# Optimization experiments

Measured on AMD Instinct MI355X. Metric: run time of the kernel, lower is better.

The kernel has to match this reference:

```python
import jax, jax.numpy as jnp
import numpy as np

TEMPERATURE = 0.5
EPS = 1e-20


def setup_inputs() -> dict:
    key = jax.random.key(0)
    ks = jax.random.split(key, 7)
    N, T, S = 16, 64, 1024
    SRC, TGT, D = 512, 512, 64
    return {
        "input": jax.random.normal(ks[0], (N, T, TGT), jnp.float32),
        "memory_bank": jax.random.normal(ks[1], (N, S, SRC), jnp.float32),
        "W_q": jax.random.normal(ks[2], (TGT, D), jnp.float32) / np.sqrt(TGT),
        "W_ctx": jax.random.normal(ks[3], (SRC, D), jnp.float32) / np.sqrt(SRC),
        "v": jax.random.normal(ks[4], (D,), jnp.float32) / np.sqrt(D),
        "W_out": jax.random.normal(ks[5], (SRC + TGT, TGT), jnp.float32) / np.sqrt(SRC + TGT),
        "b_out": jax.random.normal(ks[6], (TGT,), jnp.float32) * 0.01,
    }


def reference(input, memory_bank, W_q, W_ctx, v, W_out, b_out):
    # MLP attention score: v^T tanh(W_q q + W_ctx h)
    wq = jnp.einsum("ntd,de->nte", input, W_q)            # [N,T,D]
    uh = jnp.einsum("nsd,de->nse", memory_bank, W_ctx)    # [N,S,D]
    wquh = jnp.tanh(wq[:, :, None, :] + uh[:, None, :, :])  # [N,T,S,D]
    scores = jnp.einsum("ntsd,d->nts", wquh, v)           # [N,T,S]

    log_alpha = jax.nn.log_softmax(scores, axis=-1)
    alpha = jnp.exp(log_alpha)                            # c_align_vectors

    # deterministic context + output
    context_c = jnp.einsum("nts,nsd->ntd", alpha, memory_bank)
    h_c = jnp.tanh(jnp.concatenate([input, context_c], axis=-1) @ W_out + b_out)

    # gumbel-softmax sample (K = n_samples = 1, forced by view_as in original)
    u = jax.random.uniform(jax.random.key(42), log_alpha.shape, jnp.float32)
    g = -jnp.log(-jnp.log(u + EPS) + EPS)                 # gumbel noise
    y_align = jax.nn.softmax((log_alpha + g) / TEMPERATURE, axis=-1)  # [N,T,S]

    context_y = jnp.einsum("nts,nsd->ntd", y_align, memory_bank)
    h_y = jnp.tanh(jnp.concatenate([input, context_y], axis=-1) @ W_out + b_out)

    return jnp.stack([h_c, h_y], axis=0)  # [2,N,T,tgt_dim]
```

## Files before the change

### kernel.cpp

```cpp
#include <hip/hip_runtime.h>
#include <hip/hip_bf16.h>
#include <stdint.h>

#define DEV __device__ __forceinline__

typedef __attribute__((ext_vector_type(8))) short short8;
typedef __attribute__((ext_vector_type(4))) float f32x4;

#define TWO_LOG2E 2.8853900817779268f

DEV unsigned short f2bf(float f) {
  uint32_t u = __float_as_uint(f);
  u += 0x7FFFu + ((u >> 16) & 1u);
  return (unsigned short)(u >> 16);
}

DEV uint2 pk4(float4 f) {
  union { __hip_bfloat162 h; unsigned u; } a, b;
  a.h = __float22bfloat162_rn(make_float2(f.x, f.y));
  b.h = __float22bfloat162_rn(make_float2(f.z, f.w));
  return make_uint2(a.u, b.u);
}

DEV short8 mk8(uint2 lo, uint2 hi) {
  union { short8 s; uint4 u; } t;
  t.u = make_uint4(lo.x, lo.y, hi.x, hi.y);
  return t.s;
}

DEV uint32_t rotl32(uint32_t x, int r) { return (x << r) | (x >> (32 - r)); }

DEV void threefry_0_42(uint32_t x0, uint32_t x1, uint32_t& o0, uint32_t& o1) {
  const uint32_t ks0 = 0u, ks1 = 42u, ks2 = 0x1BD11BDAu ^ 42u;
  x0 += ks0; x1 += ks1;
#define TFR(r) { x0 += x1; x1 = rotl32(x1, (r)); x1 ^= x0; }
  TFR(13) TFR(15) TFR(26) TFR(6)  x0 += ks1; x1 += ks2 + 1u;
  TFR(17) TFR(29) TFR(16) TFR(24) x0 += ks2; x1 += ks0 + 2u;
  TFR(13) TFR(15) TFR(26) TFR(6)  x0 += ks0; x1 += ks1 + 3u;
  TFR(17) TFR(29) TFR(16) TFR(24) x0 += ks1; x1 += ks2 + 4u;
  TFR(13) TFR(15) TFR(26) TFR(6)  x0 += ks2; x1 += ks0 + 5u;
#undef TFR
  o0 = x0; o1 = x1;
}

DEV float wredmax(float v) {
#pragma unroll
  for (int off = 32; off > 0; off >>= 1) v = fmaxf(v, __shfl_xor(v, off));
  return v;
}
DEV float wredsum(float v) {
#pragma unroll
  for (int off = 32; off > 0; off >>= 1) v += __shfl_xor(v, off);
  return v;
}

__global__ __launch_bounds__(256) void transpose_all(const float* __restrict__ Wctx,
                                                     const float* __restrict__ Wq,
                                                     const float* __restrict__ Wout,
                                                     unsigned short* __restrict__ WctxT,
                                                     unsigned short* __restrict__ WqT,
                                                     unsigned short* __restrict__ WoutT) {
  __shared__ float tile[64][65];
  const int b = blockIdx.x;
  const float* src; unsigned short* dst; int R, C, br, bc;
  if (b < 8)       { src = Wctx; dst = WctxT; R = 512;  C = 64;  br = b * 64;        bc = 0; }
  else if (b < 16) { src = Wq;   dst = WqT;   R = 512;  C = 64;  br = (b - 8) * 64;  bc = 0; }
  else { int i = b - 16; src = Wout; dst = WoutT; R = 1024; C = 512; br = (i & 15) * 64; bc = (i >> 4) * 64; }
  const int tid = threadIdx.x;
  const int lr = tid >> 4, lc4 = (tid & 15) * 4;
#pragma unroll
  for (int i = 0; i < 4; ++i) {
    float4 v = *(const float4*)(src + (long)(br + lr + i * 16) * C + bc + lc4);
    tile[lr + i * 16][lc4 + 0] = v.x;
    tile[lr + i * 16][lc4 + 1] = v.y;
    tile[lr + i * 16][lc4 + 2] = v.z;
    tile[lr + i * 16][lc4 + 3] = v.w;
  }
  __syncthreads();
#pragma unroll
  for (int i = 0; i < 4; ++i) {
    int crow = lr + i * 16;
    ushort4 o;
    o.x = f2bf(tile[lc4 + 0][crow]);
    o.y = f2bf(tile[lc4 + 1][crow]);
    o.z = f2bf(tile[lc4 + 2][crow]);
    o.w = f2bf(tile[lc4 + 3][crow]);
    *(ushort4*)(dst + (long)(bc + crow) * R + br + lc4) = o;
  }
}

__global__ __launch_bounds__(256) void gemm_uhwq(const float* __restrict__ mb,
                                                 const float* __restrict__ input,
                                                 const unsigned short* __restrict__ WctxT,
                                                 const unsigned short* __restrict__ WqT,
                                                 float* __restrict__ uh,
                                                 float* __restrict__ wqo) {
  __shared__ unsigned short As[64][32];
  __shared__ unsigned short Bs[64][32];
  const int tid = threadIdx.x;
  const int bx = blockIdx.x;
  const float* A;  const unsigned short* BT;  float* C;  int mbase;
  if (bx < 256) { A = mb;    BT = WctxT; C = uh;  mbase = bx * 64; }
  else          { A = input; BT = WqT;   C = wqo; mbase = (bx - 256) * 64; }
  const int srow = tid >> 2, kc = tid & 3;
  const int scol = ((kc ^ (srow & 3)) * 8);
  const int wave = tid >> 6, lane = tid & 63;
  const int wm = (wave >> 1) * 32, wn = (wave & 1) * 32;
  const int q = lane >> 4, r = lane & 15;
  const int c0 = ((q ^ (r & 3)) * 8);
  const float* ap = A + (long)(mbase + srow) * 512 + kc * 8;
  const unsigned short* bp = BT + (long)srow * 512 + kc * 8;
  f32x4 acc[2][2];
#pragma unroll
  for (int i = 0; i < 2; ++i)
#pragma unroll
    for (int j = 0; j < 2; ++j) acc[i][j] = (f32x4){0.f, 0.f, 0.f, 0.f};

  float4 fa0 = *(const float4*)(ap);
  float4 fa1 = *(const float4*)(ap + 4);
  uint4 fb = *(const uint4*)(bp);
  for (int k0 = 0; k0 < 512; k0 += 32) {
    uint2 p0 = pk4(fa0), p1 = pk4(fa1);
    *(uint4*)&As[srow][scol] = make_uint4(p0.x, p0.y, p1.x, p1.y);
    *(uint4*)&Bs[srow][scol] = fb;
    __syncthreads();
    if (k0 + 32 < 512) {
      fa0 = *(const float4*)(ap + k0 + 32);
      fa1 = *(const float4*)(ap + k0 + 36);
      fb = *(const uint4*)(bp + k0 + 32);
    }
    short8 a0 = *(const short8*)&As[wm + r][c0];
    short8 a1 = *(const short8*)&As[wm + 16 + r][c0];
    short8 b0 = *(const short8*)&Bs[wn + r][c0];
    short8 b1 = *(const short8*)&Bs[wn + 16 + r][c0];
    acc[0][0] = __builtin_amdgcn_mfma_f32_16x16x32_bf16(a0, b0, acc[0][0], 0, 0, 0);
    acc[0][1] = __builtin_amdgcn_mfma_f32_16x16x32_bf16(a0, b1, acc[0][1], 0, 0, 0);
    acc[1][0] = __builtin_amdgcn_mfma_f32_16x16x32_bf16(a1, b0, acc[1][0], 0, 0, 0);
    acc[1][1] = __builtin_amdgcn_mfma_f32_16x16x32_bf16(a1, b1, acc[1][1], 0, 0, 0);
    __syncthreads();
  }
#pragma unroll
  for (int i2 = 0; i2 < 2; ++i2)
#pragma unroll
    for (int j2 = 0; j2 < 2; ++j2) {
      int gcol = wn + j2 * 16 + r;
#pragma unroll
      for (int reg = 0; reg < 4; ++reg) {
        int grow = mbase + wm + i2 * 16 + q * 4 + reg;
        C[(long)grow * 64 + gcol] = acc[i2][j2][reg] * TWO_LOG2E;
      }
    }
}

__global__ __launch_bounds__(256) void gemm_ctx_mfma(const float* __restrict__ alpha,
                                                     const float* __restrict__ yal,
                                                     const float* __restrict__ mb,
                                                     float* __restrict__ ctx) {
  __shared__ unsigned short As[64][32];
  const int tid = threadIdx.x;
  const int vt = blockIdx.x >> 4, n = blockIdx.x & 15;
  const int dbase = blockIdx.y * 32;
  const int srow = tid >> 2, kc = tid & 3;
  const int scol = ((kc ^ (srow & 3)) * 8);
  const int wave = tid >> 6, lane = tid & 63;
  const int wm = (wave >> 1) * 32, wn = (wave & 1) * 16;
  const int q = lane >> 4, r = lane & 15;
  const int c0 = ((q ^ (r & 3)) * 8);
  const float* Abase = (vt == 0 ? alpha : yal) + (long)n * 65536;
  const float* ap = Abase + (long)srow * 1024 + kc * 8;
  const float* bcol = mb + (long)n * 524288 + dbase + wn + r;
  f32x4 acc[2];
  acc[0] = (f32x4){0.f, 0.f, 0.f, 0.f};
  acc[1] = (f32x4){0.f, 0.f, 0.f, 0.f};

  float4 fa0 = *(const float4*)(ap);
  float4 fa1 = *(const float4*)(ap + 4);
  float bv[8];
#pragma unroll
  for (int j = 0; j < 8; ++j) bv[j] = bcol[(long)(q * 8 + j) * 512];

  for (int k0 = 0; k0 < 1024; k0 += 32) {
    uint2 p0 = pk4(fa0), p1 = pk4(fa1);
    *(uint4*)&As[srow][scol] = make_uint4(p0.x, p0.y, p1.x, p1.y);
    __syncthreads();
    float4 blo = make_float4(bv[0], bv[1], bv[2], bv[3]);
    float4 bhi = make_float4(bv[4], bv[5], bv[6], bv[7]);
    short8 b0 = mk8(pk4(blo), pk4(bhi));
    if (k0 + 32 < 1024) {
      fa0 = *(const float4*)(ap + k0 + 32);
      fa1 = *(const float4*)(ap + k0 + 36);
#pragma unroll
      for (int j = 0; j < 8; ++j) bv[j] = bcol[(long)(k0 + 32 + q * 8 + j) * 512];
    }
    short8 a0 = *(const short8*)&As[wm + r][c0];
    short8 a1 = *(const short8*)&As[wm + 16 + r][c0];
    acc[0] = __builtin_amdgcn_mfma_f32_16x16x32_bf16(a0, b0, acc[0], 0, 0, 0);
    acc[1] = __builtin_amdgcn_mfma_f32_16x16x32_bf16(a1, b0, acc[1], 0, 0, 0);
    __syncthreads();
  }
#pragma unroll
  for (int i2 = 0; i2 < 2; ++i2) {
    int gcol = dbase + wn + r;
#pragma unroll
    for (int reg = 0; reg < 4; ++reg) {
      long grow = (long)vt * 1024 + n * 64 + wm + i2 * 16 + q * 4 + reg;
      ctx[grow * 512 + gcol] = acc[i2][reg];
    }
  }
}

__global__ __launch_bounds__(256) void gemm_out_mfma(const float* __restrict__ input,
                                                     const float* __restrict__ ctx,
                                                     const unsigned short* __restrict__ WoutT,
                                                     const float* __restrict__ bout,
                                                     float* __restrict__ out) {
  __shared__ unsigned short As[64][32];
  __shared__ unsigned short Bs[64][32];
  const int tid = threadIdx.x;
  const int mbase = blockIdx.x * 64, nbase = blockIdx.y * 64;
  const int srow = tid >> 2, kc = tid & 3;
  const int scol = ((kc ^ (srow & 3)) * 8);
  const int wave = tid >> 6, lane = tid & 63;
  const int wm = (wave >> 1) * 32, wn = (wave & 1) * 32;
  const int q = lane >> 4, r = lane & 15;
  const int c0 = ((q ^ (r & 3)) * 8);
  const int vv = mbase >> 10, nt = (mbase + srow) & 1023;
  const float* ap_lo = input + (long)nt * 512 + kc * 8;
  const float* ap_hi = ctx + (long)(vv * 1024 + nt) * 512 + kc * 8 - 512;
  const unsigned short* bp = WoutT + (long)(nbase + srow) * 1024 + kc * 8;
  f32x4 acc[2][2];
#pragma unroll
  for (int i = 0; i < 2; ++i)
#pragma unroll
    for (int j = 0; j < 2; ++j) acc[i][j] = (f32x4){0.f, 0.f, 0.f, 0.f};

  float4 fa0 = *(const float4*)(ap_lo);
  float4 fa1 = *(const float4*)(ap_lo + 4);
  uint4 fb = *(const uint4*)(bp);
  for (int k0 = 0; k0 < 1024; k0 += 32) {
    uint2 p0 = pk4(fa0), p1 = pk4(fa1);
    *(uint4*)&As[srow][scol] = make_uint4(p0.x, p0.y, p1.x, p1.y);
    *(uint4*)&Bs[srow][scol] = fb;
    __syncthreads();
    int kn = k0 + 32;
    if (kn < 1024) {
      const float* apn = (kn < 512) ? ap_lo : ap_hi;
      fa0 = *(const float4*)(apn + kn);
      fa1 = *(const float4*)(apn + kn + 4);
      fb = *(const uint4*)(bp + kn);
    }
    short8 a0 = *(const short8*)&As[wm + r][c0];
    short8 a1 = *(const short8*)&As[wm + 16 + r][c0];
    short8 b0 = *(const short8*)&Bs[wn + r][c0];
    short8 b1 = *(const short8*)&Bs[wn + 16 + r][c0];
    acc[0][0] = __builtin_amdgcn_mfma_f32_16x16x32_bf16(a0, b0, acc[0][0], 0, 0, 0);
    acc[0][1] = __builtin_amdgcn_mfma_f32_16x16x32_bf16(a0, b1, acc[0][1], 0, 0, 0);
    acc[1][0] = __builtin_amdgcn_mfma_f32_16x16x32_bf16(a1, b0, acc[1][0], 0, 0, 0);
    acc[1][1] = __builtin_amdgcn_mfma_f32_16x16x32_bf16(a1, b1, acc[1][1], 0, 0, 0);
    __syncthreads();
  }
#pragma unroll
  for (int i2 = 0; i2 < 2; ++i2)
#pragma unroll
    for (int j2 = 0; j2 < 2; ++j2) {
      int gcol = nbase + wn + j2 * 16 + r;
      float bb = bout[gcol];
#pragma unroll
      for (int reg = 0; reg < 4; ++reg) {
        int grow = mbase + wm + i2 * 16 + q * 4 + reg;
        float z = acc[i2][j2][reg] + bb;
        float rc = __builtin_amdgcn_rcpf(1.f + __builtin_amdgcn_exp2f(z * TWO_LOG2E));
        out[(long)grow * 512 + gcol] = fmaf(-2.f, rc, 1.f);
      }
    }
}

__global__ __launch_bounds__(256) void scores_kernel(const float* __restrict__ uh2,
                                                     const float* __restrict__ wq2,
                                                     const float* __restrict__ v,
                                                     float* __restrict__ alpha_g,
                                                     float* __restrict__ y_g) {
  const int tid = threadIdx.x;
  const int nt = blockIdx.x;
  const int n = nt >> 6;
  __shared__ float wvs[64];
  __shared__ float vvs[64];
  __shared__ float red[4];
  if (tid < 64) {
    wvs[tid] = wq2[nt * 64 + tid];
    vvs[tid] = v[tid];
  }
  __syncthreads();

  float sumv = 0.f;
#pragma unroll
  for (int d = 0; d < 64; d += 4) {
    float4 vv = *(const float4*)&vvs[d];
    sumv += vv.x + vv.y + vv.z + vv.w;
  }

  const float* un = uh2 + (long)n * 65536;
  float lsc[4];
#pragma unroll
  for (int i = 0; i < 4; ++i) {
    const float* up = un + (long)(i * 256 + tid) * 64;
    float racc = 0.f;
#pragma unroll
    for (int dc = 0; dc < 16; ++dc) {
      float4 u = *(const float4*)(up + dc * 4);
      float4 w = *(const float4*)&wvs[dc * 4];
      float4 vv = *(const float4*)&vvs[dc * 4];
      racc = fmaf(vv.x, __builtin_amdgcn_rcpf(1.f + __builtin_amdgcn_exp2f(u.x + w.x)), racc);
      racc = fmaf(vv.y, __builtin_amdgcn_rcpf(1.f + __builtin_amdgcn_exp2f(u.y + w.y)), racc);
      racc = fmaf(vv.z, __builtin_amdgcn_rcpf(1.f + __builtin_amdgcn_exp2f(u.z + w.z)), racc);
      racc = fmaf(vv.w, __builtin_amdgcn_rcpf(1.f + __builtin_amdgcn_exp2f(u.w + w.w)), racc);
    }
    lsc[i] = fmaf(-2.f, racc, sumv);
  }

  const int wv = tid >> 6, ln = tid & 63;
  float m = fmaxf(fmaxf(lsc[0], lsc[1]), fmaxf(lsc[2], lsc[3]));
  m = wredmax(m);
  if (ln == 0) red[wv] = m;
  __syncthreads();
  m = fmaxf(fmaxf(red[0], red[1]), fmaxf(red[2], red[3]));
  __syncthreads();
  float ss = 0.f;
#pragma unroll
  for (int i = 0; i < 4; ++i) ss += __expf(lsc[i] - m);
  ss = wredsum(ss);
  if (ln == 0) red[wv] = ss;
  __syncthreads();
  ss = red[0] + red[1] + red[2] + red[3];
  const float logl = __logf(ss);
  __syncthreads();

  float ys[4];
#pragma unroll
  for (int i = 0; i < 4; ++i) {
    int s = tid + 256 * i;
    float la = lsc[i] - m - logl;
    alpha_g[(long)nt * 1024 + s] = __expf(la);
    uint32_t j = (uint32_t)nt * 1024u + (uint32_t)s;
    uint32_t o0, o1;
    threefry_0_42(0u, j, o0, o1);
    uint32_t bits = o0 ^ o1;
    float u = __uint_as_float((bits >> 9) | 0x3f800000u) - 1.0f;
    float g = -__logf(-__logf(u + 1e-20f) + 1e-20f);
    ys[i] = (la + g) * 2.0f;
  }

  float m2 = fmaxf(fmaxf(ys[0], ys[1]), fmaxf(ys[2], ys[3]));
  m2 = wredmax(m2);
  if (ln == 0) red[wv] = m2;
  __syncthreads();
  m2 = fmaxf(fmaxf(red[0], red[1]), fmaxf(red[2], red[3]));
  __syncthreads();
  float s2 = 0.f;
  float ye[4];
#pragma unroll
  for (int i = 0; i < 4; ++i) { ye[i] = __expf(ys[i] - m2); s2 += ye[i]; }
  s2 = wredsum(s2);
  if (ln == 0) red[wv] = s2;
  __syncthreads();
  s2 = red[0] + red[1] + red[2] + red[3];
  const float rinv = __fdividef(1.f, s2);
#pragma unroll
  for (int i = 0; i < 4; ++i) y_g[(long)nt * 1024 + tid + 256 * i] = ye[i] * rinv;
}

extern "C" void kernel_launch(void* const* d_in, const int* in_sizes, int n_in,
                              void* d_out, int out_size, void* d_ws, size_t ws_size,
                              hipStream_t stream) {
  const float* input = (const float*)d_in[0];
  const float* mb    = (const float*)d_in[1];
  const float* W_q   = (const float*)d_in[2];
  const float* W_ctx = (const float*)d_in[3];
  const float* v     = (const float*)d_in[4];
  const float* W_out = (const float*)d_in[5];
  const float* b_out = (const float*)d_in[6];
  float* out = (float*)d_out;
  float* ws = (float*)d_ws;

  float* uh    = ws;
  float* wq    = ws + 1048576;
  float* yal   = ws + 1114112;
  unsigned short* WctxT = (unsigned short*)(ws + 2162688);
  unsigned short* WqT   = (unsigned short*)(ws + 2179072);
  unsigned short* WoutT = (unsigned short*)(ws + 2195456);
  float* alpha = out;
  float* ctx   = uh;

  transpose_all<<<144, 256, 0, stream>>>(W_ctx, W_q, W_out, WctxT, WqT, WoutT);
  gemm_uhwq<<<272, 256, 0, stream>>>(mb, input, WctxT, WqT, uh, wq);
  scores_kernel<<<1024, 256, 0, stream>>>(uh, wq, v, alpha, yal);
  gemm_ctx_mfma<<<dim3(32, 16), 256, 0, stream>>>(alpha, yal, mb, ctx);
  gemm_out_mfma<<<dim3(32, 8), 256, 0, stream>>>(input, ctx, WoutT, b_out, out);
}
```

Baseline: 177.6 us.

## Store uh transposed for coalesced score reads and halve output GEMM N-tile

The uh GEMM now writes its result transposed as [N][D][S], so the scores kernel can have each thread handle four consecutive s positions. Each d-row then becomes a coalesced float4 load, replacing the strided per-row reads of 64 floats. The alpha and y writes become float4 stores, and the threefry counters are remapped to match. Separately, the output GEMM uses a 32-wide N tile with a doubled grid to raise the block count, at the cost of more A-tile reloads and idle B-loading threads.

```diff
diff --git a/kernel.cpp b/kernel.cpp
--- a/kernel.cpp
+++ b/kernel.cpp
@@ -93,15 +93,15 @@
                                                  const float* __restrict__ input,
                                                  const unsigned short* __restrict__ WctxT,
                                                  const unsigned short* __restrict__ WqT,
-                                                 float* __restrict__ uh,
+                                                 float* __restrict__ uhT,
                                                  float* __restrict__ wqo) {
   __shared__ unsigned short As[64][32];
   __shared__ unsigned short Bs[64][32];
   const int tid = threadIdx.x;
   const int bx = blockIdx.x;
-  const float* A;  const unsigned short* BT;  float* C;  int mbase;
-  if (bx < 256) { A = mb;    BT = WctxT; C = uh;  mbase = bx * 64; }
-  else          { A = input; BT = WqT;   C = wqo; mbase = (bx - 256) * 64; }
+  const float* A;  const unsigned short* BT;  int mbase;
+  if (bx < 256) { A = mb;    BT = WctxT; mbase = bx * 64; }
+  else          { A = input; BT = WqT;   mbase = (bx - 256) * 64; }
   const int srow = tid >> 2, kc = tid & 3;
   const int scol = ((kc ^ (srow & 3)) * 8);
   const int wave = tid >> 6, lane = tid & 63;
@@ -144,10 +144,19 @@
 #pragma unroll
     for (int j2 = 0; j2 < 2; ++j2) {
       int gcol = wn + j2 * 16 + r;
-#pragma unroll
-      for (int reg = 0; reg < 4; ++reg) {
-        int grow = mbase + wm + i2 * 16 + q * 4 + reg;
-        C[(long)grow * 64 + gcol] = acc[i2][j2][reg] * TWO_LOG2E;
+      int m = mbase + wm + i2 * 16 + q * 4;
+      if (bx < 256) {
+        int n = m >> 10, s0 = m & 1023;
+        float4 o;
+        o.x = acc[i2][j2][0] * TWO_LOG2E;
+        o.y = acc[i2][j2][1] * TWO_LOG2E;
+        o.z = acc[i2][j2][2] * TWO_LOG2E;
+        o.w = acc[i2][j2][3] * TWO_LOG2E;
+        *(float4*)(uhT + (long)n * 65536 + (long)gcol * 1024 + s0) = o;
+      } else {
+#pragma unroll
+        for (int reg = 0; reg < 4; ++reg)
+          wqo[(long)(m + reg) * 64 + gcol] = acc[i2][j2][reg] * TWO_LOG2E;
       }
     }
 }
@@ -215,67 +224,62 @@
                                                      const float* __restrict__ bout,
                                                      float* __restrict__ out) {
   __shared__ unsigned short As[64][32];
-  __shared__ unsigned short Bs[64][32];
+  __shared__ unsigned short Bs[32][32];
   const int tid = threadIdx.x;
-  const int mbase = blockIdx.x * 64, nbase = blockIdx.y * 64;
+  const int mbase = blockIdx.x * 64, nbase = blockIdx.y * 32;
   const int srow = tid >> 2, kc = tid & 3;
   const int scol = ((kc ^ (srow & 3)) * 8);
   const int wave = tid >> 6, lane = tid & 63;
-  const int wm = (wave >> 1) * 32, wn = (wave & 1) * 32;
+  const int wm = (wave >> 1) * 32, wn = (wave & 1) * 16;
   const int q = lane >> 4, r = lane & 15;
   const int c0 = ((q ^ (r & 3)) * 8);
   const int vv = mbase >> 10, nt = (mbase + srow) & 1023;
   const float* ap_lo = input + (long)nt * 512 + kc * 8;
   const float* ap_hi = ctx + (long)(vv * 1024 + nt) * 512 + kc * 8 - 512;
-  const unsigned short* bp = WoutT + (long)(nbase + srow) * 1024 + kc * 8;
-  f32x4 acc[2][2];
-#pragma unroll
-  for (int i = 0; i < 2; ++i)
-#pragma unroll
-    for (int j = 0; j < 2; ++j) acc[i][j] = (f32x4){0.f, 0.f, 0.f, 0.f};
+  const int brow = (tid & 127) >> 2;
+  const unsigned short* bp = WoutT + (long)(nbase + brow) * 1024 + kc * 8;
+  f32x4 acc[2];
+  acc[0] = (f32x4){0.f, 0.f, 0.f, 0.f};
+  acc[1] = (f32x4){0.f, 0.f, 0.f, 0.f};
 
   float4 fa0 = *(const float4*)(ap_lo);
   float4 fa1 = *(const float4*)(ap_lo + 4);
-  uint4 fb = *(const uint4*)(bp);
+  uint4 fb;
+  if (tid < 128) fb = *(const uint4*)(bp);
   for (int k0 = 0; k0 < 1024; k0 += 32) {
     uint2 p0 = pk4(fa0), p1 = pk4(fa1);
     *(uint4*)&As[srow][scol] = make_uint4(p0.x, p0.y, p1.x, p1.y);
-    *(uint4*)&Bs[srow][scol] = fb;
+    if (tid < 128) *(uint4*)&Bs[brow][(kc ^ (brow & 3)) * 8] = fb;
     __syncthreads();
     int kn = k0 + 32;
     if (kn < 1024) {
       const float* apn = (kn < 512) ? ap_lo : ap_hi;
       fa0 = *(const float4*)(apn + kn);
       fa1 = *(const float4*)(apn + kn + 4);
-      fb = *(const uint4*)(bp + kn);
+      if (tid < 128) fb = *(const uint4*)(bp + kn);
     }
     short8 a0 = *(const short8*)&As[wm + r][c0];
     short8 a1 = *(const short8*)&As[wm + 16 + r][c0];
     short8 b0 = *(const short8*)&Bs[wn + r][c0];
-    short8 b1 = *(const short8*)&Bs[wn + 16 + r][c0];
-    acc[0][0] = __builtin_amdgcn_mfma_f32_16x16x32_bf16(a0, b0, acc[0][0], 0, 0, 0);
-    acc[0][1] = __builtin_amdgcn_mfma_f32_16x16x32_bf16(a0, b1, acc[0][1], 0, 0, 0);
-    acc[1][0] = __builtin_amdgcn_mfma_f32_16x16x32_bf16(a1, b0, acc[1][0], 0, 0, 0);
-    acc[1][1] = __builtin_amdgcn_mfma_f32_16x16x32_bf16(a1, b1, acc[1][1], 0, 0, 0);
-    __syncthreads();
-  }
-#pragma unroll
-  for (int i2 = 0; i2 < 2; ++i2)
-#pragma unroll
-    for (int j2 = 0; j2 < 2; ++j2) {
-      int gcol = nbase + wn + j2 * 16 + r;
-      float bb = bout[gcol];
-#pragma unroll
-      for (int reg = 0; reg < 4; ++reg) {
-        int grow = mbase + wm + i2 * 16 + q * 4 + reg;
-        float z = acc[i2][j2][reg] + bb;
-        float rc = __builtin_amdgcn_rcpf(1.f + __builtin_amdgcn_exp2f(z * TWO_LOG2E));
-        out[(long)grow * 512 + gcol] = fmaf(-2.f, rc, 1.f);
-      }
-    }
-}
-
-__global__ __launch_bounds__(256) void scores_kernel(const float* __restrict__ uh2,
+    acc[0] = __builtin_amdgcn_mfma_f32_16x16x32_bf16(a0, b0, acc[0], 0, 0, 0);
+    acc[1] = __builtin_amdgcn_mfma_f32_16x16x32_bf16(a1, b0, acc[1], 0, 0, 0);
+    __syncthreads();
+  }
+#pragma unroll
+  for (int i2 = 0; i2 < 2; ++i2) {
+    int gcol = nbase + wn + r;
+    float bb = bout[gcol];
+#pragma unroll
+    for (int reg = 0; reg < 4; ++reg) {
+      int grow = mbase + wm + i2 * 16 + q * 4 + reg;
+      float z = acc[i2][reg] + bb;
+      float rc = __builtin_amdgcn_rcpf(1.f + __builtin_amdgcn_exp2f(z * TWO_LOG2E));
+      out[(long)grow * 512 + gcol] = fmaf(-2.f, rc, 1.f);
+    }
+  }
+}
+
+__global__ __launch_bounds__(256) void scores_kernel(const float* __restrict__ uhT,
                                                      const float* __restrict__ wq2,
                                                      const float* __restrict__ v,
                                                      float* __restrict__ alpha_g,
@@ -299,24 +303,26 @@
     sumv += vv.x + vv.y + vv.z + vv.w;
   }
 
-  const float* un = uh2 + (long)n * 65536;
+  const float* un = uhT + (long)n * 65536 + tid * 4;
+  float4 racc = make_float4(0.f, 0.f, 0.f, 0.f);
+  for (int db = 0; db < 64; db += 8) {
+    float4 ub[8];
+#pragma unroll
+    for (int j = 0; j < 8; ++j) ub[j] = *(const float4*)(un + (long)(db + j) * 1024);
+#pragma unroll
+    for (int j = 0; j < 8; ++j) {
+      float w = wvs[db + j], vvj = vvs[db + j];
+      racc.x = fmaf(vvj, __builtin_amdgcn_rcpf(1.f + __builtin_amdgcn_exp2f(ub[j].x + w)), racc.x);
+      racc.y = fmaf(vvj, __builtin_amdgcn_rcpf(1.f + __builtin_amdgcn_exp2f(ub[j].y + w)), racc.y);
+      racc.z = fmaf(vvj, __builtin_amdgcn_rcpf(1.f + __builtin_amdgcn_exp2f(ub[j].z + w)), racc.z);
+      racc.w = fmaf(vvj, __builtin_amdgcn_rcpf(1.f + __builtin_amdgcn_exp2f(ub[j].w + w)), racc.w);
+    }
+  }
   float lsc[4];
-#pragma unroll
-  for (int i = 0; i < 4; ++i) {
-    const float* up = un + (long)(i * 256 + tid) * 64;
-    float racc = 0.f;
-#pragma unroll
-    for (int dc = 0; dc < 16; ++dc) {
-      float4 u = *(const float4*)(up + dc * 4);
-      float4 w = *(const float4*)&wvs[dc * 4];
-      float4 vv = *(const float4*)&vvs[dc * 4];
-      racc = fmaf(vv.x, __builtin_amdgcn_rcpf(1.f + __builtin_amdgcn_exp2f(u.x + w.x)), racc);
-      racc = fmaf(vv.y, __builtin_amdgcn_rcpf(1.f + __builtin_amdgcn_exp2f(u.y + w.y)), racc);
-      racc = fmaf(vv.z, __builtin_amdgcn_rcpf(1.f + __builtin_amdgcn_exp2f(u.z + w.z)), racc);
-      racc = fmaf(vv.w, __builtin_amdgcn_rcpf(1.f + __builtin_amdgcn_exp2f(u.w + w.w)), racc);
-    }
-    lsc[i] = fmaf(-2.f, racc, sumv);
-  }
+  lsc[0] = fmaf(-2.f, racc.x, sumv);
+  lsc[1] = fmaf(-2.f, racc.y, sumv);
+  lsc[2] = fmaf(-2.f, racc.z, sumv);
+  lsc[3] = fmaf(-2.f, racc.w, sumv);
 
   const int wv = tid >> 6, ln = tid & 63;
   float m = fmaxf(fmaxf(lsc[0], lsc[1]), fmaxf(lsc[2], lsc[3]));
@@ -335,20 +341,21 @@
   const float logl = __logf(ss);
   __syncthreads();
 
+  const uint32_t jbase = (uint32_t)nt * 1024u + (uint32_t)tid * 4u;
   float ys[4];
+  float4 av;
 #pragma unroll
   for (int i = 0; i < 4; ++i) {
-    int s = tid + 256 * i;
     float la = lsc[i] - m - logl;
-    alpha_g[(long)nt * 1024 + s] = __expf(la);
-    uint32_t j = (uint32_t)nt * 1024u + (uint32_t)s;
+    ((float*)&av)[i] = __expf(la);
     uint32_t o0, o1;
-    threefry_0_42(0u, j, o0, o1);
+    threefry_0_42(0u, jbase + i, o0, o1);
     uint32_t bits = o0 ^ o1;
     float u = __uint_as_float((bits >> 9) | 0x3f800000u) - 1.0f;
     float g = -__logf(-__logf(u + 1e-20f) + 1e-20f);
     ys[i] = (la + g) * 2.0f;
   }
+  *(float4*)(alpha_g + (long)nt * 1024 + tid * 4) = av;
 
   float m2 = fmaxf(fmaxf(ys[0], ys[1]), fmaxf(ys[2], ys[3]));
   m2 = wredmax(m2);
@@ -357,16 +364,16 @@
   m2 = fmaxf(fmaxf(red[0], red[1]), fmaxf(red[2], red[3]));
   __syncthreads();
   float s2 = 0.f;
-  float ye[4];
-#pragma unroll
-  for (int i = 0; i < 4; ++i) { ye[i] = __expf(ys[i] - m2); s2 += ye[i]; }
+  float4 ye;
+#pragma unroll
+  for (int i = 0; i < 4; ++i) { ((float*)&ye)[i] = __expf(ys[i] - m2); s2 += ((float*)&ye)[i]; }
   s2 = wredsum(s2);
   if (ln == 0) red[wv] = s2;
   __syncthreads();
   s2 = red[0] + red[1] + red[2] + red[3];
   const float rinv = __fdividef(1.f, s2);
-#pragma unroll
-  for (int i = 0; i < 4; ++i) y_g[(long)nt * 1024 + tid + 256 * i] = ye[i] * rinv;
+  ye.x *= rinv; ye.y *= rinv; ye.z *= rinv; ye.w *= rinv;
+  *(float4*)(y_g + (long)nt * 1024 + tid * 4) = ye;
 }
 
 extern "C" void kernel_launch(void* const* d_in, const int* in_sizes, int n_in,
@@ -382,18 +389,18 @@
   float* out = (float*)d_out;
   float* ws = (float*)d_ws;
 
-  float* uh    = ws;
+  float* uhT   = ws;
   float* wq    = ws + 1048576;
   float* yal   = ws + 1114112;
   unsigned short* WctxT = (unsigned short*)(ws + 2162688);
   unsigned short* WqT   = (unsigned short*)(ws + 2179072);
   unsigned short* WoutT = (unsigned short*)(ws + 2195456);
   float* alpha = out;
-  float* ctx   = uh;
+  float* ctx   = uhT;
 
   transpose_all<<<144, 256, 0, stream>>>(W_ctx, W_q, W_out, WctxT, WqT, WoutT);
-  gemm_uhwq<<<272, 256, 0, stream>>>(mb, input, WctxT, WqT, uh, wq);
-  scores_kernel<<<1024, 256, 0, stream>>>(uh, wq, v, alpha, yal);
+  gemm_uhwq<<<272, 256, 0, stream>>>(mb, input, WctxT, WqT, uhT, wq);
+  scores_kernel<<<1024, 256, 0, stream>>>(uhT, wq, v, alpha, yal);
   gemm_ctx_mfma<<<dim3(32, 16), 256, 0, stream>>>(alpha, yal, mb, ctx);
-  gemm_out_mfma<<<dim3(32, 8), 256, 0, stream>>>(input, ctx, WoutT, b_out, out);
-}
+  gemm_out_mfma<<<dim3(32, 16), 256, 0, stream>>>(input, ctx, WoutT, b_out, out);
+}
```

New measurement: 153.6 us. 1.16x faster.
